# Kernel optimization log

Measured on AMD Instinct MI355X. Metric: run time of the kernel, lower is better.

## Reference

```python
import jax, jax.numpy as jnp
import numpy as np

B, D, K = 256, 1024, 128  # batch, num variables (leaves), units per node


def setup_inputs() -> dict:
    key = jax.random.key(0)
    k1, k2, k3, k4 = jax.random.split(key, 4)
    x = jax.random.normal(k1, (B, D), dtype=jnp.float32)
    mu = jax.random.normal(k2, (D, K), dtype=jnp.float32)
    log_sigma = 0.1 * jax.random.normal(k3, (D, K), dtype=jnp.float32)
    # log-weight logits for all 512+256+...+1 = 1023 inner sum nodes, concatenated
    weights = jax.random.normal(k4, (D - 1, K, K), dtype=jnp.float32)
    return {"x": x, "mu": mu, "log_sigma": log_sigma, "weights": weights}


def _log_matmul(y, logw):
    # y: [B, d, K] log-values; logw: [d, K, K] normalized log-weights (<= 0)
    # out[b,d,i] = logsumexp_j( logw[d,i,j] + y[b,d,j] ), computed without
    # materializing a [B,d,K,K] tensor: shift-by-max + linear-space matmul.
    m = jnp.max(y, axis=-1, keepdims=True)                  # [B, d, 1]
    e = jnp.exp(y - m)                                      # [B, d, K]
    s = jnp.einsum("bdj,dij->bdi", e, jnp.exp(logw))        # [B, d, K]
    return m + jnp.log(s)


def reference(x, mu, log_sigma, weights):
    # --- input (leaf) layer: per-variable Gaussian log-densities, [B, D, K] ---
    half_log_2pi = 0.5 * jnp.log(jnp.asarray(2.0 * np.pi, dtype=x.dtype))
    z = (x[:, :, None] - mu) * jnp.exp(-log_sigma)
    y = -0.5 * z * z - log_sigma - half_log_2pi             # [B, D, K]

    # --- topological sweep over the binary-tree DAG: product then sum layers ---
    off = 0
    d = y.shape[1]
    while d > 1:
        d //= 2
        # product nodes: sum log-probs of adjacent children -> [B, d, K]
        y = y[:, 0::2, :] + y[:, 1::2, :]
        # sum nodes: normalized log-space mixture over K child units
        logw = jax.nn.log_softmax(weights[off:off + d], axis=-1)  # [d, K, K]
        y = _log_matmul(y, logw)
        off += d
    return y[:, 0, :]  # root outputs, [B, K]
```

## Files before the change

kernel.cpp:

```cpp
#include <hip/hip_runtime.h>
#include <math.h>


#define DD 1024
#define KK 128
#define HALF_LOG_2PI 0.9189385332046727f

typedef __attribute__((ext_vector_type(8))) short bf16x8;
typedef __attribute__((ext_vector_type(4))) float f32x4;

__device__ __forceinline__ unsigned short bf16_rn(float f) {
    unsigned u = __builtin_bit_cast(unsigned, f);
    u += 0x7fffu + ((u >> 16) & 1u);
    return (unsigned short)(u >> 16);
}
__device__ __forceinline__ float bf16f(unsigned short h) {
    unsigned u = ((unsigned)h) << 16;
    return __builtin_bit_cast(float, u);
}

template <int BT, int NTH, bool LEAF>
__global__ __launch_bounds__(NTH, 4) void spn_level(
    const float* __restrict__ x, const float* __restrict__ mu,
    const float* __restrict__ ls, const float* __restrict__ yprev,
    const float* __restrict__ weights, float* __restrict__ yout,
    int d, int woff)
{
    constexpr int NW  = NTH / 64;
    constexpr int NRT = BT / 16;
    constexpr int WPR = NW / NRT;
    constexpr int NCI = 8 / WPR;

    extern __shared__ char smem[];
    unsigned short* Whi = (unsigned short*)smem;
    unsigned short* Wlo = Whi + 16384;
    float* logrs = (float*)(Wlo + 16384);
    float* musig = logrs + 128;

    const int n     = blockIdx.x;
    const int btile = blockIdx.y;
    const int t     = threadIdx.x;
    const int node  = woff + n;

    {
        constexpr int TPR = NTH / 128;
        constexpr int EPT = 128 / TPR;
        const int i = t / TPR, h = t % TPR;
        const float* wr = weights + ((size_t)node << 14) + i * 128 + h * EPT;
        unsigned short* wh = Whi + i * 128;
        unsigned short* wl = Wlo + i * 128;
        const int sw = (i & 7) << 3;
        float ps = 0.f;
        #pragma unroll
        for (int c = 0; c < EPT / 8; ++c) {
            float4 v0 = *(const float4*)(wr + 8 * c);
            float4 v1 = *(const float4*)(wr + 8 * c + 4);
            float e[8] = {__expf(v0.x), __expf(v0.y), __expf(v0.z), __expf(v0.w),
                          __expf(v1.x), __expf(v1.y), __expf(v1.z), __expf(v1.w)};
            bf16x8 hv, lv;
            #pragma unroll
            for (int q = 0; q < 8; ++q) {
                ps += e[q];
                const unsigned short hb = bf16_rn(e[q]);
                hv[q] = (short)hb;
                lv[q] = (short)bf16_rn(e[q] - bf16f(hb));
            }
            const int j0 = h * EPT + 8 * c;
            *(bf16x8*)&wh[j0 ^ sw] = hv;
            *(bf16x8*)&wl[j0 ^ sw] = lv;
        }
        #pragma unroll
        for (int s2 = 1; s2 < TPR; s2 <<= 1) ps += __shfl_xor(ps, s2);
        if (h == 0) logrs[i] = __logf(ps);
    }
    if (LEAF && t < 256) {
        const int c = t >> 7, j = t & 127;
        const float lsv = ls[(size_t)(2 * n + c) * KK + j];
        musig[c * 128 + j]       = __expf(-lsv);
        musig[256 + c * 128 + j] = -lsv - HALF_LOG_2PI;
        musig[512 + c * 128 + j] = mu[(size_t)(2 * n + c) * KK + j];
    }
    __syncthreads();

    const int w  = t >> 6;
    const int ln = t & 63;
    const int lr = ln & 15;
    const int lk = ln >> 4;
    const int rt  = w / WPR;
    const int ci0 = (w % WPR) * NCI;
    const int brow = btile * BT + rt * 16 + lr;

    float p[32];
    if (LEAF) {
        const float xa = x[(size_t)brow * DD + 2 * n];
        const float xb = x[(size_t)brow * DD + 2 * n + 1];
        #pragma unroll
        for (int ks = 0; ks < 4; ++ks) {
            #pragma unroll
            for (int g = 0; g < 2; ++g) {
                const int j = ks * 32 + lk * 8 + 4 * g;
                const float4 ia = *(const float4*)&musig[j];
                const float4 ib = *(const float4*)&musig[128 + j];
                const float4 ca = *(const float4*)&musig[256 + j];
                const float4 cb = *(const float4*)&musig[384 + j];
                const float4 ma = *(const float4*)&musig[512 + j];
                const float4 mb = *(const float4*)&musig[640 + j];
                float za, zb;
                za = (xa - ma.x) * ia.x; zb = (xb - mb.x) * ib.x;
                p[ks * 8 + 4 * g + 0] = fmaf(-0.5f * za, za, ca.x) + fmaf(-0.5f * zb, zb, cb.x);
                za = (xa - ma.y) * ia.y; zb = (xb - mb.y) * ib.y;
                p[ks * 8 + 4 * g + 1] = fmaf(-0.5f * za, za, ca.y) + fmaf(-0.5f * zb, zb, cb.y);
                za = (xa - ma.z) * ia.z; zb = (xb - mb.z) * ib.z;
                p[ks * 8 + 4 * g + 2] = fmaf(-0.5f * za, za, ca.z) + fmaf(-0.5f * zb, zb, cb.z);
                za = (xa - ma.w) * ia.w; zb = (xb - mb.w) * ib.w;
                p[ks * 8 + 4 * g + 3] = fmaf(-0.5f * za, za, ca.w) + fmaf(-0.5f * zb, zb, cb.w);
            }
        }
    } else {
        const float* ra = yprev + ((size_t)brow * (2 * d) + 2 * n) * KK;
        #pragma unroll
        for (int ks = 0; ks < 4; ++ks) {
            const int j0 = ks * 32 + lk * 8;
            const float4 a0 = *(const float4*)(ra + j0);
            const float4 a1 = *(const float4*)(ra + j0 + 4);
            const float4 b0 = *(const float4*)(ra + KK + j0);
            const float4 b1 = *(const float4*)(ra + KK + j0 + 4);
            p[ks * 8 + 0] = a0.x + b0.x; p[ks * 8 + 1] = a0.y + b0.y;
            p[ks * 8 + 2] = a0.z + b0.z; p[ks * 8 + 3] = a0.w + b0.w;
            p[ks * 8 + 4] = a1.x + b1.x; p[ks * 8 + 5] = a1.y + b1.y;
            p[ks * 8 + 6] = a1.z + b1.z; p[ks * 8 + 7] = a1.w + b1.w;
        }
    }

    float m16[16];
    #pragma unroll
    for (int q = 0; q < 16; ++q) m16[q] = fmaxf(p[q], p[q + 16]);
    float m8[8];
    #pragma unroll
    for (int q = 0; q < 8; ++q) m8[q] = fmaxf(m16[q], m16[q + 8]);
    float m4a[4];
    #pragma unroll
    for (int q = 0; q < 4; ++q) m4a[q] = fmaxf(m8[q], m8[q + 4]);
    float mx = fmaxf(fmaxf(m4a[0], m4a[1]), fmaxf(m4a[2], m4a[3]));
    mx = fmaxf(mx, __shfl_xor(mx, 16));
    mx = fmaxf(mx, __shfl_xor(mx, 32));

    bf16x8 ah[4], al[4];
    #pragma unroll
    for (int ks = 0; ks < 4; ++ks) {
        #pragma unroll
        for (int q = 0; q < 8; ++q) {
            const float ev = __expf(p[ks * 8 + q] - mx);
            const unsigned short hb = bf16_rn(ev);
            ah[ks][q] = (short)hb;
            al[ks][q] = (short)bf16_rn(ev - bf16f(hb));
        }
    }

    f32x4 acc[NCI];
    #pragma unroll
    for (int ci = 0; ci < NCI; ++ci) acc[ci] = (f32x4){0.f, 0.f, 0.f, 0.f};
    #pragma unroll
    for (int ci = 0; ci < NCI; ++ci) {
        const int i = (ci0 + ci) * 16 + lr;
        const int base = i * 128;
        const int sw = (i & 7) << 3;
        #pragma unroll
        for (int ks = 0; ks < 4; ++ks) {
            const int idx = base + ((ks * 32 + lk * 8) ^ sw);
            const bf16x8 bh = *(bf16x8*)&Whi[idx];
            const bf16x8 bl = *(bf16x8*)&Wlo[idx];
            acc[ci] = __builtin_amdgcn_mfma_f32_16x16x32_bf16(ah[ks], bh, acc[ci], 0, 0, 0);
            acc[ci] = __builtin_amdgcn_mfma_f32_16x16x32_bf16(ah[ks], bl, acc[ci], 0, 0, 0);
            acc[ci] = __builtin_amdgcn_mfma_f32_16x16x32_bf16(al[ks], bh, acc[ci], 0, 0, 0);
        }
    }

    float mv4[4];
    #pragma unroll
    for (int r = 0; r < 4; ++r) mv4[r] = __shfl(mx, lk * 4 + r);
    #pragma unroll
    for (int ci = 0; ci < NCI; ++ci) {
        const int icol = (ci0 + ci) * 16 + lr;
        const float lrsv = logrs[icol];
        #pragma unroll
        for (int r = 0; r < 4; ++r) {
            const int b = btile * BT + rt * 16 + lk * 4 + r;
            yout[((size_t)b * d + n) * KK + icol] = mv4[r] + __logf(acc[ci][r]) - lrsv;
        }
    }
}

extern "C" void kernel_launch(void* const* d_in, const int* in_sizes, int n_in,
                              void* d_out, int out_size, void* d_ws, size_t ws_size,
                              hipStream_t stream) {
    const float* x  = (const float*)d_in[0];
    const float* mu = (const float*)d_in[1];
    const float* ls = (const float*)d_in[2];
    const float* w  = (const float*)d_in[3];
    float* out  = (float*)d_out;
    float* buf0 = (float*)d_ws;
    float* buf1 = buf0 + (size_t)256 * 512 * KK;

    const int shBig   = 65536 + 512 + 3072;
    const int shSmall = 65536 + 512;

    (void)hipFuncSetAttribute((const void*)spn_level<128, 512, true>,
                              hipFuncAttributeMaxDynamicSharedMemorySize, shBig);
    (void)hipFuncSetAttribute((const void*)spn_level<128, 512, false>,
                              hipFuncAttributeMaxDynamicSharedMemorySize, shBig);
    (void)hipFuncSetAttribute((const void*)spn_level<32, 256, false>,
                              hipFuncAttributeMaxDynamicSharedMemorySize, shSmall);

    spn_level<128, 512, true><<<dim3(512, 2), dim3(512), shBig, stream>>>(
        x, mu, ls, nullptr, w, buf0, 512, 0);

    const float* src = buf0;
    float* other = buf1;
    int woff = 512;
    for (int d = 256; d >= 1; d >>= 1) {
        float* o = (d == 1) ? out : other;
        if (d >= 64) {
            spn_level<128, 512, false><<<dim3(d, 2), dim3(512), shBig, stream>>>(
                nullptr, nullptr, nullptr, src, w, o, d, woff);
        } else {
            spn_level<32, 256, false><<<dim3(d, 8), dim3(256), shSmall, stream>>>(
                nullptr, nullptr, nullptr, src, w, o, d, woff);
        }
        woff += d;
        other = (float*)src;
        src = o;
    }
}
```

Baseline: 245.3 us.

## Carry linear-space values with per-row scale and fuse last five levels

Intermediate levels now store linear-space mixture outputs plus a per-row log-scale instead of log values. This replaces the exp/log pair per element with a multiply and one log per row, and folds weight normalisation into the bf16 planes. The levels with d=16..1 are fused into a single tail kernel that keeps intermediates in shared memory, using weight planes precomputed by a small pre-pass. This removes five kernel launches and the log/exp overhead, but trades away some dynamic range because products of linear values can underflow, guarded only by a 1e-30 floor.

```diff
diff --git a/kernel.cpp b/kernel.cpp
--- a/kernel.cpp
+++ b/kernel.cpp
@@ -19,23 +19,59 @@
     return __builtin_bit_cast(float, u);
 }
 
-template <int BT, int NTH, bool LEAF>
-__global__ __launch_bounds__(NTH, 4) void spn_level(
+__global__ __launch_bounds__(256) void w_pre_tail(
+    const float* __restrict__ weights, unsigned short* __restrict__ planes)
+{
+    __shared__ float red[256];
+    const int nl = blockIdx.x;
+    const int t = threadIdx.x;
+    const int i = t >> 1, h = t & 1;
+    const float* wg = weights + (((size_t)(992 + nl)) << 14) + (i << 7) + (h << 6);
+    float ev[64];
+    float ps = 0.f;
+    #pragma unroll
+    for (int q = 0; q < 16; ++q) {
+        const float4 v = *(const float4*)(wg + 4 * q);
+        ev[4 * q + 0] = __expf(v.x); ev[4 * q + 1] = __expf(v.y);
+        ev[4 * q + 2] = __expf(v.z); ev[4 * q + 3] = __expf(v.w);
+        ps += (ev[4 * q + 0] + ev[4 * q + 1]) + (ev[4 * q + 2] + ev[4 * q + 3]);
+    }
+    red[t] = ps;
+    __syncthreads();
+    const float rinv = 1.f / (red[2 * i] + red[2 * i + 1]);
+    unsigned short* wh = planes + ((size_t)nl << 15) + (i << 7);
+    unsigned short* wl = wh + 16384;
+    const int sw = (i & 7) << 3;
+    #pragma unroll
+    for (int c = 0; c < 8; ++c) {
+        bf16x8 hv, lv;
+        #pragma unroll
+        for (int q = 0; q < 8; ++q) {
+            const float e = ev[8 * c + q] * rinv;
+            const unsigned short hb = bf16_rn(e);
+            hv[q] = (short)hb;
+            lv[q] = (short)bf16_rn(e - bf16f(hb));
+        }
+        const int j0 = (h << 6) + 8 * c;
+        *(bf16x8*)&wh[j0 ^ sw] = hv;
+        *(bf16x8*)&wl[j0 ^ sw] = lv;
+    }
+}
+
+template <int BT, bool LEAF>
+__global__ __launch_bounds__(512, 4) void spn_level(
     const float* __restrict__ x, const float* __restrict__ mu,
-    const float* __restrict__ ls, const float* __restrict__ yprev,
-    const float* __restrict__ weights, float* __restrict__ yout,
+    const float* __restrict__ ls, const float* __restrict__ Ein,
+    const float* __restrict__ Min, const float* __restrict__ weights,
+    float* __restrict__ Eout, float* __restrict__ Mout,
     int d, int woff)
 {
-    constexpr int NW  = NTH / 64;
-    constexpr int NRT = BT / 16;
-    constexpr int WPR = NW / NRT;
-    constexpr int NCI = 8 / WPR;
+    constexpr int NW = 8, NRT = BT / 16, WPR = NW / NRT, NCI = 8 / WPR;
 
     extern __shared__ char smem[];
     unsigned short* Whi = (unsigned short*)smem;
     unsigned short* Wlo = Whi + 16384;
-    float* logrs = (float*)(Wlo + 16384);
-    float* musig = logrs + 128;
+    float* musig = (float*)(Wlo + 16384);
 
     const int n     = blockIdx.x;
     const int btile = blockIdx.y;
@@ -43,35 +79,37 @@
     const int node  = woff + n;
 
     {
-        constexpr int TPR = NTH / 128;
-        constexpr int EPT = 128 / TPR;
-        const int i = t / TPR, h = t % TPR;
-        const float* wr = weights + ((size_t)node << 14) + i * 128 + h * EPT;
-        unsigned short* wh = Whi + i * 128;
-        unsigned short* wl = Wlo + i * 128;
+        const int i = t >> 2, h = t & 3;
+        const float* wr = weights + ((size_t)node << 14) + (i << 7) + (h << 5);
+        float ev[32];
+        float ps = 0.f;
+        #pragma unroll
+        for (int q = 0; q < 8; ++q) {
+            const float4 v = *(const float4*)(wr + 4 * q);
+            ev[4 * q + 0] = __expf(v.x); ev[4 * q + 1] = __expf(v.y);
+            ev[4 * q + 2] = __expf(v.z); ev[4 * q + 3] = __expf(v.w);
+            ps += (ev[4 * q + 0] + ev[4 * q + 1]) + (ev[4 * q + 2] + ev[4 * q + 3]);
+        }
+        ps += __shfl_xor(ps, 1);
+        ps += __shfl_xor(ps, 2);
+        const float rinv = 1.f / ps;
         const int sw = (i & 7) << 3;
-        float ps = 0.f;
-        #pragma unroll
-        for (int c = 0; c < EPT / 8; ++c) {
-            float4 v0 = *(const float4*)(wr + 8 * c);
-            float4 v1 = *(const float4*)(wr + 8 * c + 4);
-            float e[8] = {__expf(v0.x), __expf(v0.y), __expf(v0.z), __expf(v0.w),
-                          __expf(v1.x), __expf(v1.y), __expf(v1.z), __expf(v1.w)};
+        unsigned short* wh = Whi + (i << 7);
+        unsigned short* wl = Wlo + (i << 7);
+        #pragma unroll
+        for (int c = 0; c < 4; ++c) {
             bf16x8 hv, lv;
             #pragma unroll
             for (int q = 0; q < 8; ++q) {
-                ps += e[q];
-                const unsigned short hb = bf16_rn(e[q]);
+                const float e = ev[8 * c + q] * rinv;
+                const unsigned short hb = bf16_rn(e);
                 hv[q] = (short)hb;
-                lv[q] = (short)bf16_rn(e[q] - bf16f(hb));
-            }
-            const int j0 = h * EPT + 8 * c;
+                lv[q] = (short)bf16_rn(e - bf16f(hb));
+            }
+            const int j0 = (h << 5) + 8 * c;
             *(bf16x8*)&wh[j0 ^ sw] = hv;
             *(bf16x8*)&wl[j0 ^ sw] = lv;
         }
-        #pragma unroll
-        for (int s2 = 1; s2 < TPR; s2 <<= 1) ps += __shfl_xor(ps, s2);
-        if (h == 0) logrs[i] = __logf(ps);
     }
     if (LEAF && t < 256) {
         const int c = t >> 7, j = t & 127;
@@ -91,6 +129,7 @@
     const int brow = btile * BT + rt * 16 + lr;
 
     float p[32];
+    float M2;
     if (LEAF) {
         const float xa = x[(size_t)brow * DD + 2 * n];
         const float xb = x[(size_t)brow * DD + 2 * n + 1];
@@ -117,7 +156,7 @@
             }
         }
     } else {
-        const float* ra = yprev + ((size_t)brow * (2 * d) + 2 * n) * KK;
+        const float* ra = Ein + ((size_t)brow * (2 * d) + 2 * n) * KK;
         #pragma unroll
         for (int ks = 0; ks < 4; ++ks) {
             const int j0 = ks * 32 + lk * 8;
@@ -125,10 +164,10 @@
             const float4 a1 = *(const float4*)(ra + j0 + 4);
             const float4 b0 = *(const float4*)(ra + KK + j0);
             const float4 b1 = *(const float4*)(ra + KK + j0 + 4);
-            p[ks * 8 + 0] = a0.x + b0.x; p[ks * 8 + 1] = a0.y + b0.y;
-            p[ks * 8 + 2] = a0.z + b0.z; p[ks * 8 + 3] = a0.w + b0.w;
-            p[ks * 8 + 4] = a1.x + b1.x; p[ks * 8 + 5] = a1.y + b1.y;
-            p[ks * 8 + 6] = a1.z + b1.z; p[ks * 8 + 7] = a1.w + b1.w;
+            p[ks * 8 + 0] = a0.x * b0.x; p[ks * 8 + 1] = a0.y * b0.y;
+            p[ks * 8 + 2] = a0.z * b0.z; p[ks * 8 + 3] = a0.w * b0.w;
+            p[ks * 8 + 4] = a1.x * b1.x; p[ks * 8 + 5] = a1.y * b1.y;
+            p[ks * 8 + 6] = a1.z * b1.z; p[ks * 8 + 7] = a1.w * b1.w;
         }
     }
 
@@ -146,15 +185,32 @@
     mx = fmaxf(mx, __shfl_xor(mx, 32));
 
     bf16x8 ah[4], al[4];
-    #pragma unroll
-    for (int ks = 0; ks < 4; ++ks) {
-        #pragma unroll
-        for (int q = 0; q < 8; ++q) {
-            const float ev = __expf(p[ks * 8 + q] - mx);
-            const unsigned short hb = bf16_rn(ev);
-            ah[ks][q] = (short)hb;
-            al[ks][q] = (short)bf16_rn(ev - bf16f(hb));
-        }
+    if (LEAF) {
+        M2 = mx;
+        #pragma unroll
+        for (int ks = 0; ks < 4; ++ks)
+            #pragma unroll
+            for (int q = 0; q < 8; ++q) {
+                const float ev = __expf(p[ks * 8 + q] - mx);
+                const unsigned short hb = bf16_rn(ev);
+                ah[ks][q] = (short)hb;
+                al[ks][q] = (short)bf16_rn(ev - bf16f(hb));
+            }
+    } else {
+        const float mg = fmaxf(mx, 1e-30f);
+        const float rinv = 1.f / mg;
+        const float Ma = Min[(size_t)brow * (2 * d) + 2 * n];
+        const float Mb = Min[(size_t)brow * (2 * d) + 2 * n + 1];
+        M2 = Ma + Mb + __logf(mg);
+        #pragma unroll
+        for (int ks = 0; ks < 4; ++ks)
+            #pragma unroll
+            for (int q = 0; q < 8; ++q) {
+                const float ev = p[ks * 8 + q] * rinv;
+                const unsigned short hb = bf16_rn(ev);
+                ah[ks][q] = (short)hb;
+                al[ks][q] = (short)bf16_rn(ev - bf16f(hb));
+            }
     }
 
     f32x4 acc[NCI];
@@ -176,19 +232,165 @@
         }
     }
 
-    float mv4[4];
-    #pragma unroll
-    for (int r = 0; r < 4; ++r) mv4[r] = __shfl(mx, lk * 4 + r);
-    #pragma unroll
-    for (int ci = 0; ci < NCI; ++ci) {
-        const int icol = (ci0 + ci) * 16 + lr;
-        const float lrsv = logrs[icol];
-        #pragma unroll
-        for (int r = 0; r < 4; ++r) {
-            const int b = btile * BT + rt * 16 + lk * 4 + r;
-            yout[((size_t)b * d + n) * KK + icol] = mv4[r] + __logf(acc[ci][r]) - lrsv;
-        }
-    }
+    #pragma unroll
+    for (int r = 0; r < 4; ++r) {
+        const int b = btile * BT + rt * 16 + lk * 4 + r;
+        #pragma unroll
+        for (int ci = 0; ci < NCI; ++ci)
+            Eout[((size_t)b * d + n) * KK + (ci0 + ci) * 16 + lr] = acc[ci][r];
+    }
+    if (ln < 16 && ci0 == 0)
+        Mout[(size_t)(btile * BT + rt * 16 + ln) * d + n] = M2;
+}
+
+template <int NOUT, bool GIN, bool GOUT>
+__device__ __forceinline__ void tail_level(
+    const float* __restrict__ gE, const float* __restrict__ gM,
+    const float* __restrict__ lE, const float* __restrict__ lM,
+    float* __restrict__ oE, float* __restrict__ oM, float* __restrict__ gOut,
+    const unsigned short* __restrict__ planes, int planeBase, int blk, int t)
+{
+    constexpr int NN    = 2 * NOUT;
+    constexpr int REP   = (NOUT >= 8) ? NOUT / 8 : 1;
+    constexpr int SHARE = (NOUT >= 8) ? 1 : 8 / NOUT;
+    constexpr int NCI   = 8 / SHARE;
+    const int w  = t >> 6;
+    const int ln = t & 63;
+    const int lr = ln & 15;
+    const int lk = ln >> 4;
+    const int row = lr & 3;
+    const bool vrow = (lr < 4);
+    const int node0 = (NOUT >= 8) ? w * REP : w / SHARE;
+    const int ci0   = (NOUT >= 8) ? 0 : (w % SHARE) * NCI;
+
+    #pragma unroll
+    for (int rep = 0; rep < REP; ++rep) {
+        const int nd = node0 + rep;
+        float p[32];
+        #pragma unroll
+        for (int ks = 0; ks < 4; ++ks) {
+            #pragma unroll
+            for (int hf = 0; hf < 2; ++hf) {
+                const int k = ks * 32 + lk * 8 + hf * 4;
+                float4 ea, eb;
+                if constexpr (GIN) {
+                    const float* base = gE + ((size_t)(blk * 4 + row) * NN + 2 * nd) * KK + k;
+                    ea = *(const float4*)base;
+                    eb = *(const float4*)(base + KK);
+                } else {
+                    const int scj = (k >> 2) ^ ((row & 3) << 1);
+                    ea = *(const float4*)&lE[(row * NN + 2 * nd) * KK + (scj << 2)];
+                    eb = *(const float4*)&lE[(row * NN + 2 * nd + 1) * KK + (scj << 2)];
+                }
+                const int o = ks * 8 + hf * 4;
+                p[o + 0] = vrow ? ea.x * eb.x : 0.f;
+                p[o + 1] = vrow ? ea.y * eb.y : 0.f;
+                p[o + 2] = vrow ? ea.z * eb.z : 0.f;
+                p[o + 3] = vrow ? ea.w * eb.w : 0.f;
+            }
+        }
+        float m16[16];
+        #pragma unroll
+        for (int q = 0; q < 16; ++q) m16[q] = fmaxf(p[q], p[q + 16]);
+        float m8[8];
+        #pragma unroll
+        for (int q = 0; q < 8; ++q) m8[q] = fmaxf(m16[q], m16[q + 8]);
+        float m4a[4];
+        #pragma unroll
+        for (int q = 0; q < 4; ++q) m4a[q] = fmaxf(m8[q], m8[q + 4]);
+        float mx = fmaxf(fmaxf(m4a[0], m4a[1]), fmaxf(m4a[2], m4a[3]));
+        mx = fmaxf(mx, __shfl_xor(mx, 16));
+        mx = fmaxf(mx, __shfl_xor(mx, 32));
+        const float mg = fmaxf(mx, 1e-30f);
+        const float rinv = 1.f / mg;
+        float Ma, Mb;
+        if constexpr (GIN) {
+            Ma = gM[(size_t)(blk * 4 + row) * NN + 2 * nd];
+            Mb = gM[(size_t)(blk * 4 + row) * NN + 2 * nd + 1];
+        } else {
+            Ma = lM[row * NN + 2 * nd];
+            Mb = lM[row * NN + 2 * nd + 1];
+        }
+        const float M2 = Ma + Mb + __logf(mg);
+
+        bf16x8 ah[4], al[4];
+        #pragma unroll
+        for (int ks = 0; ks < 4; ++ks)
+            #pragma unroll
+            for (int q = 0; q < 8; ++q) {
+                const float ev = p[ks * 8 + q] * rinv;
+                const unsigned short hb = bf16_rn(ev);
+                ah[ks][q] = (short)hb;
+                al[ks][q] = (short)bf16_rn(ev - bf16f(hb));
+            }
+
+        f32x4 acc[NCI];
+        #pragma unroll
+        for (int ci = 0; ci < NCI; ++ci) acc[ci] = (f32x4){0.f, 0.f, 0.f, 0.f};
+        #pragma unroll
+        for (int ci = 0; ci < NCI; ++ci) {
+            const int wrow = (ci0 + ci) * 16 + lr;
+            const int swr = (wrow & 7) << 3;
+            const unsigned short* ph = planes + (((size_t)(planeBase + nd)) << 15) + wrow * KK;
+            #pragma unroll
+            for (int ks = 0; ks < 4; ++ks) {
+                const int k = (ks * 32 + lk * 8) ^ swr;
+                const bf16x8 bh = *(const bf16x8*)&ph[k];
+                const bf16x8 bl = *(const bf16x8*)&ph[16384 + k];
+                acc[ci] = __builtin_amdgcn_mfma_f32_16x16x32_bf16(ah[ks], bh, acc[ci], 0, 0, 0);
+                acc[ci] = __builtin_amdgcn_mfma_f32_16x16x32_bf16(ah[ks], bl, acc[ci], 0, 0, 0);
+                acc[ci] = __builtin_amdgcn_mfma_f32_16x16x32_bf16(al[ks], bh, acc[ci], 0, 0, 0);
+            }
+        }
+
+        if constexpr (GOUT) {
+            float mr[4];
+            #pragma unroll
+            for (int r = 0; r < 4; ++r) mr[r] = __shfl(M2, r);
+            if (lk == 0) {
+                #pragma unroll
+                for (int r = 0; r < 4; ++r)
+                    #pragma unroll
+                    for (int ci = 0; ci < NCI; ++ci)
+                        gOut[(size_t)(blk * 4 + r) * KK + (ci0 + ci) * 16 + lr] =
+                            mr[r] + __logf(acc[ci][r]);
+            }
+        } else {
+            if (lk == 0) {
+                #pragma unroll
+                for (int r = 0; r < 4; ++r) {
+                    #pragma unroll
+                    for (int ci = 0; ci < NCI; ++ci) {
+                        const int icol = (ci0 + ci) * 16 + lr;
+                        const int scj = (icol >> 2) ^ ((r & 3) << 1);
+                        oE[(r * NOUT + nd) * KK + (scj << 2) + (icol & 3)] = acc[ci][r];
+                    }
+                }
+            }
+            if (ln < 4 && ci0 == 0) oM[ln * NOUT + nd] = M2;
+        }
+    }
+}
+
+__global__ __launch_bounds__(512, 4) void spn_tail(
+    const float* __restrict__ E32, const float* __restrict__ M32,
+    const unsigned short* __restrict__ planes, float* __restrict__ out)
+{
+    __shared__ float SA[4 * 16 * KK];
+    __shared__ float SB[4 * 8 * KK];
+    __shared__ float MA[4 * 16];
+    __shared__ float MB2[4 * 8];
+    const int blk = blockIdx.x;
+    const int t   = threadIdx.x;
+    tail_level<16, true,  false>(E32, M32, nullptr, nullptr, SA, MA, nullptr, planes, 0,  blk, t);
+    __syncthreads();
+    tail_level<8,  false, false>(nullptr, nullptr, SA, MA, SB, MB2, nullptr, planes, 16, blk, t);
+    __syncthreads();
+    tail_level<4,  false, false>(nullptr, nullptr, SB, MB2, SA, MA, nullptr, planes, 24, blk, t);
+    __syncthreads();
+    tail_level<2,  false, false>(nullptr, nullptr, SA, MA, SB, MB2, nullptr, planes, 28, blk, t);
+    __syncthreads();
+    tail_level<1,  false, true >(nullptr, nullptr, SB, MB2, nullptr, nullptr, out, planes, 30, blk, t);
 }
 
 extern "C" void kernel_launch(void* const* d_in, const int* in_sizes, int n_in,
@@ -201,34 +403,30 @@
     float* out  = (float*)d_out;
     float* buf0 = (float*)d_ws;
     float* buf1 = buf0 + (size_t)256 * 512 * KK;
-
-    const int shBig   = 65536 + 512 + 3072;
-    const int shSmall = 65536 + 512;
-
-    (void)hipFuncSetAttribute((const void*)spn_level<128, 512, true>,
-                              hipFuncAttributeMaxDynamicSharedMemorySize, shBig);
-    (void)hipFuncSetAttribute((const void*)spn_level<128, 512, false>,
-                              hipFuncAttributeMaxDynamicSharedMemorySize, shBig);
-    (void)hipFuncSetAttribute((const void*)spn_level<32, 256, false>,
-                              hipFuncAttributeMaxDynamicSharedMemorySize, shSmall);
-
-    spn_level<128, 512, true><<<dim3(512, 2), dim3(512), shBig, stream>>>(
-        x, mu, ls, nullptr, w, buf0, 512, 0);
-
-    const float* src = buf0;
-    float* other = buf1;
-    int woff = 512;
-    for (int d = 256; d >= 1; d >>= 1) {
-        float* o = (d == 1) ? out : other;
-        if (d >= 64) {
-            spn_level<128, 512, false><<<dim3(d, 2), dim3(512), shBig, stream>>>(
-                nullptr, nullptr, nullptr, src, w, o, d, woff);
-        } else {
-            spn_level<32, 256, false><<<dim3(d, 8), dim3(256), shSmall, stream>>>(
-                nullptr, nullptr, nullptr, src, w, o, d, woff);
-        }
-        woff += d;
-        other = (float*)src;
-        src = o;
-    }
-}
+    float* M0   = buf1 + (size_t)256 * 256 * KK;
+    float* M1   = M0 + 256 * 512;
+    unsigned short* planes = (unsigned short*)(M1 + 256 * 256);
+
+    const int shA = 65536 + 3072;
+
+    (void)hipFuncSetAttribute((const void*)spn_level<128, true>,
+                              hipFuncAttributeMaxDynamicSharedMemorySize, shA);
+    (void)hipFuncSetAttribute((const void*)spn_level<128, false>,
+                              hipFuncAttributeMaxDynamicSharedMemorySize, shA);
+    (void)hipFuncSetAttribute((const void*)spn_level<32, false>,
+                              hipFuncAttributeMaxDynamicSharedMemorySize, shA);
+
+    w_pre_tail<<<dim3(31), dim3(256), 0, stream>>>(w, planes);
+
+    spn_level<128, true><<<dim3(512, 2), dim3(512), shA, stream>>>(
+        x, mu, ls, nullptr, nullptr, w, buf0, M0, 512, 0);
+    spn_level<128, false><<<dim3(256, 2), dim3(512), shA, stream>>>(
+        nullptr, nullptr, nullptr, buf0, M0, w, buf1, M1, 256, 512);
+    spn_level<128, false><<<dim3(128, 2), dim3(512), shA, stream>>>(
+        nullptr, nullptr, nullptr, buf1, M1, w, buf0, M0, 128, 768);
+    spn_level<128, false><<<dim3(64, 2), dim3(512), shA, stream>>>(
+        nullptr, nullptr, nullptr, buf0, M0, w, buf1, M1, 64, 896);
+    spn_level<32, false><<<dim3(32, 8), dim3(512), shA, stream>>>(
+        nullptr, nullptr, nullptr, buf1, M1, w, buf0, M0, 32, 960);
+    spn_tail<<<dim3(64), dim3(512), 0, stream>>>(buf0, M0, planes, out);
+}
```

Result: slower. 257.7 us (+5.1%).
